# Kernel tuning notes

Hardware: AMD Instinct MI355X
Metric: run time of the kernel (lower is better)

## Reference

```python
import jax, jax.numpy as jnp
import numpy as np

LN_EPS = 1e-5


def setup_inputs() -> dict:
    key = jax.random.key(0)
    ks = jax.random.split(key, 8)
    B, S, D = 8, 2048, 1024
    scale = 1.0 / np.sqrt(D)
    return {
        "inp": jax.random.normal(ks[0], (B, S, D), dtype=jnp.float32),
        "lens": jax.random.randint(ks[1], (B,), 1, S + 1, dtype=jnp.int64),
        "Wq": jax.random.normal(ks[2], (D, D), dtype=jnp.float32) * scale,
        "bq": jnp.zeros((D,), dtype=jnp.float32),
        "Wk": jax.random.normal(ks[3], (D, D), dtype=jnp.float32) * scale,
        "bk": jnp.zeros((D,), dtype=jnp.float32),
        "Wv": jax.random.normal(ks[4], (D, D), dtype=jnp.float32) * scale,
        "bv": jnp.zeros((D,), dtype=jnp.float32),
        "ln_gamma": jnp.ones((D,), dtype=jnp.float32),
        "ln_beta": jnp.zeros((D,), dtype=jnp.float32),
    }


def reference(inp, lens, Wq, bq, Wk, bk, Wv, bv, ln_gamma, ln_beta):
    # inp: [B, S, D]; dk = dv = D
    B, S, D = inp.shape
    q = jnp.einsum("bsd,kd->bsk", inp, Wq) + bq  # [B, S, D]
    k = jnp.einsum("bsd,kd->bsk", inp, Wk) + bk
    v = jnp.einsum("bsd,kd->bsk", inp, Wv) + bv
    # scores[b, i, j] = q[b, i] . k[b, j]
    scores = jnp.einsum("bid,bjd->bij", q, k)  # [B, S, S]
    # NON-standard: softmax over the QUERY axis (dim=1), then divide by sqrt(dk)
    attn = jax.nn.softmax(scores, axis=1) / jnp.sqrt(jnp.asarray(D, scores.dtype))
    selfatt = jnp.einsum("bij,bjd->bid", attn, v)  # [B, S, D]
    # LayerNorm over last dim, then mean-pool over sequence (sum / seq_len)
    mu = jnp.mean(selfatt, axis=-1, keepdims=True)
    var = jnp.mean(jnp.square(selfatt - mu), axis=-1, keepdims=True)
    ln = (selfatt - mu) * jax.lax.rsqrt(var + LN_EPS) * ln_gamma + ln_beta
    context = jnp.sum(ln, axis=1) / S  # [B, D]
    return context
```

## Files before the change

kernel.cpp:

```cpp
#include <hip/hip_runtime.h>
#include <hip/hip_fp16.h>

#define B_ 8
#define S_ 2048
#define D_ 1024
#define M_ (B_ * S_)
#define NCH 8
#define LN_EPS 1e-5f

typedef _Float16 f16;
typedef _Float16 half8 __attribute__((ext_vector_type(8)));
typedef _Float16 half4_t __attribute__((ext_vector_type(4)));
typedef float floatx4 __attribute__((ext_vector_type(4)));

__device__ __forceinline__ void gload_lds16(const void* g, void* l) {
  __builtin_amdgcn_global_load_lds((const __attribute__((address_space(1))) void*)g,
                                   (__attribute__((address_space(3))) void*)l, 16, 0, 0);
}

__device__ __forceinline__ void xcd_remap(int& bx, int& by, int& bz) {
  const int gx = gridDim.x, gy = gridDim.y;
  const int nb = gx * gy * (int)gridDim.z;
  int f = blockIdx.x + gx * (blockIdx.y + gy * blockIdx.z);
  const int cpx = nb >> 3;
  f = (f & 7) * cpx + (f >> 3);
  bx = f % gx;
  f /= gx;
  by = f % gy;
  bz = f / gy;
}

__global__ void k_cvt(const float* __restrict__ src, f16* __restrict__ dst, int n4) {
  int stride = gridDim.x * blockDim.x;
  for (int i = blockIdx.x * blockDim.x + threadIdx.x; i < n4; i += stride) {
    float4 v = ((const float4*)src)[i];
    half4_t h;
    h.x = (f16)v.x; h.y = (f16)v.y; h.z = (f16)v.z; h.w = (f16)v.w;
    ((half4_t*)dst)[i] = h;
  }
}

__global__ void k_cvtw(const float* __restrict__ a, const float* __restrict__ b,
                       const float* __restrict__ c, f16* __restrict__ dst) {
  const int n4 = D_ * D_ / 4;
  const int i = blockIdx.x * 256 + threadIdx.x;
  const int which = i / n4, off = i - which * n4;
  const float* s = which == 0 ? a : (which == 1 ? b : c);
  const float4 v = ((const float4*)s)[off];
  half4_t h;
  h.x = (f16)v.x; h.y = (f16)v.y; h.z = (f16)v.z; h.w = (f16)v.w;
  ((half4_t*)dst)[i] = h;
}

#define STG_A(tn, h, buf)                                                     \
  {                                                                           \
    const f16* g = aG + (size_t)(tn) * 64 + (size_t)(h) * 128 * K;            \
    f16* l = As + (buf) * 16384 + (h) * 8192 + lOff;                          \
    gload_lds16(g, l);                                                        \
    gload_lds16(g + (size_t)64 * K, l + 4096);                                \
  }
#define STG_B(tn, h, buf)                                                     \
  {                                                                           \
    const f16* g = bG + (size_t)(tn) * 64 + (size_t)(h) * 128 * K;            \
    f16* l = Bs + (buf) * 16384 + (h) * 8192 + lOff;                          \
    gload_lds16(g, l);                                                        \
    gload_lds16(g + (size_t)64 * K, l + 4096);                                \
  }

__device__ __forceinline__ void gemm8_loop(
    const f16* aG, const f16* bG, f16* As, f16* Bs, const int K, const int lOff,
    const int wr, const int wc, const int fr, const int fs0, const int fs1,
    floatx4 (&acc)[2][4][2][2]) {
  const int NT = K >> 6;
  const int NP = NT >> 1;

  STG_A(0, 0, 0);
  STG_B(0, 0, 0);
  STG_B(0, 1, 0);
  STG_A(0, 1, 0);
  STG_A(1, 0, 1);
  STG_B(1, 0, 1);
  asm volatile("s_waitcnt vmcnt(8)" ::: "memory");
  __builtin_amdgcn_s_barrier();

  half8 af[4][2], bf0[2][2], bf1[2][2];

#define LDA(BUF, MH)                                                          \
  _Pragma("unroll") for (int m = 0; m < 4; ++m) {                             \
    const f16* Ac = As + (BUF) * 16384;                                       \
    const int ar = ((MH) * 128 + wr * 64 + m * 16 + fr) * 64;                 \
    af[m][0] = *(const half8*)(Ac + ar + fs0);                                \
    af[m][1] = *(const half8*)(Ac + ar + fs1);                                \
  }
#define LDB(BUF, NH, DST)                                                     \
  _Pragma("unroll") for (int n = 0; n < 2; ++n) {                             \
    const f16* Bc = Bs + (BUF) * 16384;                                       \
    const int br = ((NH) * 128 + wc * 32 + n * 16 + fr) * 64;                 \
    DST[n][0] = *(const half8*)(Bc + br + fs0);                               \
    DST[n][1] = *(const half8*)(Bc + br + fs1);                               \
  }
#define PH(LOADS, MH, NH, BF, STAGE_STMT, WAIT_STMT)                          \
  {                                                                           \
    LOADS;                                                                    \
    STAGE_STMT;                                                               \
    __builtin_amdgcn_s_barrier();                                             \
    __builtin_amdgcn_s_setprio(1);                                            \
    _Pragma("unroll") for (int m = 0; m < 4; ++m)                             \
      _Pragma("unroll") for (int n = 0; n < 2; ++n)                           \
        _Pragma("unroll") for (int kk = 0; kk < 2; ++kk)                      \
          acc[MH][m][NH][n] = __builtin_amdgcn_mfma_f32_16x16x32_f16(         \
              af[m][kk], BF[n][kk], acc[MH][m][NH][n], 0, 0, 0);              \
    __builtin_amdgcn_s_setprio(0);                                            \
    WAIT_STMT;                                                                \
    __builtin_amdgcn_s_barrier();                                             \
  }
#define VW8 asm volatile("s_waitcnt vmcnt(8)" ::: "memory")
#define VW4 asm volatile("s_waitcnt vmcnt(4)" ::: "memory")
#define VW2 asm volatile("s_waitcnt vmcnt(2)" ::: "memory")
#define VW0 asm volatile("s_waitcnt vmcnt(0)" ::: "memory")

  for (int p = 0; p < NP; ++p) {
    const int t0 = 2 * p;
    const bool mid = (t0 + 2 < NT);
    const bool nxt = (t0 + 3 < NT);
    const bool last = (p == NP - 1);

    PH(LDA(0, 0); LDB(0, 0, bf0), 0, 0, bf0, STG_B(t0 + 1, 1, 1), VW8);
    PH(LDB(0, 1, bf1), 0, 1, bf1, STG_A(t0 + 1, 1, 1), VW8);
    PH(LDA(0, 1), 1, 1, bf1, if (mid) STG_A(t0 + 2, 0, 0), VW8);
    PH((void)0, 1, 0, bf0, if (mid) STG_B(t0 + 2, 0, 0),
       if (last) { VW4; } else { VW8; });
    PH(LDA(1, 0); LDB(1, 0, bf0), 0, 0, bf0, if (mid) STG_B(t0 + 2, 1, 0),
       if (last) { VW2; } else { VW8; });
    PH(LDB(1, 1, bf1), 0, 1, bf1, if (mid) STG_A(t0 + 2, 1, 0),
       if (last) { VW0; } else { VW8; });
    PH(LDA(1, 1), 1, 1, bf1, if (nxt) STG_A(t0 + 3, 0, 1), VW8);
    PH((void)0, 1, 0, bf0, if (nxt) STG_B(t0 + 3, 0, 1), VW8);
  }
#undef PH
#undef LDA
#undef LDB
#undef VW8
#undef VW4
#undef VW2
#undef VW0
}

template <bool OUTF16, bool BIAS>
__global__ __launch_bounds__(512, 2) void k_gemm8(
    const f16* __restrict__ A, const f16* __restrict__ Bm, void* __restrict__ Cv,
    const float* __restrict__ bias, const int K, const int N,
    const long sA, const long sB, const long sC) {
  __shared__ f16 As[2 * 256 * 64];
  __shared__ f16 Bs[2 * 256 * 64];
  int bx, by, bz;
  xcd_remap(bx, by, bz);
  const int tid = threadIdx.x;
  const int wid = tid >> 6, lane = tid & 63;
  const int wr = wid >> 2, wc = wid & 3;
  const int fr = lane & 15;

  const f16* Ab = A + (size_t)bz * sA + (size_t)by * 256 * K;
  const f16* Bb = Bm + (size_t)bz * sB + (size_t)bx * 256 * K;
  const int srow = tid >> 3;
  const int sslot = (tid & 7) ^ (srow & 7);
  const f16* aG = Ab + (size_t)srow * K + sslot * 8;
  const f16* bG = Bb + (size_t)srow * K + sslot * 8;
  const int lOff = srow * 64 + (tid & 7) * 8;

  const int sx = lane & 7;
  const int fs0 = (((lane >> 4)) ^ sx) * 8;
  const int fs1 = ((4 + (lane >> 4)) ^ sx) * 8;

  floatx4 acc[2][4][2][2] = {};
  gemm8_loop(aG, bG, As, Bs, K, lOff, wr, wc, fr, fs0, fs1, acc);

#pragma unroll
  for (int mh = 0; mh < 2; ++mh)
#pragma unroll
    for (int m = 0; m < 4; ++m) {
      const int row0 = by * 256 + mh * 128 + wr * 64 + m * 16 + (lane >> 4) * 4;
#pragma unroll
      for (int nh = 0; nh < 2; ++nh)
#pragma unroll
        for (int n = 0; n < 2; ++n) {
          const int col = bx * 256 + nh * 128 + wc * 32 + n * 16 + (lane & 15);
          float bv = 0.0f;
          if constexpr (BIAS) bv = bias[col];
#pragma unroll
          for (int r = 0; r < 4; ++r) {
            const float v = acc[mh][m][nh][n][r] + bv;
            if constexpr (OUTF16)
              ((f16*)Cv)[(size_t)bz * sC + (size_t)(row0 + r) * N + col] = (f16)v;
            else
              ((float*)Cv)[(size_t)bz * sC + (size_t)(row0 + r) * N + col] = v;
          }
        }
    }
}

__global__ __launch_bounds__(512, 2) void k_scores8(
    const f16* __restrict__ Q, const f16* __restrict__ Kx, f16* __restrict__ Sc,
    float* __restrict__ pm, float* __restrict__ pz) {
  __shared__ f16 As[2 * 256 * 64];
  __shared__ f16 Bs[2 * 256 * 64];
  __shared__ float smax[2][256];
  __shared__ float ssum[2][256];
  int bx, by, bz;
  xcd_remap(bx, by, bz);
  const int tid = threadIdx.x;
  const int wid = tid >> 6, lane = tid & 63;
  const int wr = wid >> 2, wc = wid & 3;
  const int fr = lane & 15;
  const int K = D_;

  const f16* Ab = Q + (size_t)bz * S_ * D_ + (size_t)by * 256 * K;
  const f16* Bb = Kx + (size_t)bz * S_ * D_ + (size_t)bx * 256 * K;
  const int srow = tid >> 3;
  const int sslot = (tid & 7) ^ (srow & 7);
  const f16* aG = Ab + (size_t)srow * K + sslot * 8;
  const f16* bG = Bb + (size_t)srow * K + sslot * 8;
  const int lOff = srow * 64 + (tid & 7) * 8;

  const int sx = lane & 7;
  const int fs0 = (((lane >> 4)) ^ sx) * 8;
  const int fs1 = ((4 + (lane >> 4)) ^ sx) * 8;

  floatx4 acc[2][4][2][2] = {};
  gemm8_loop(aG, bG, As, Bs, K, lOff, wr, wc, fr, fs0, fs1, acc);

#pragma unroll
  for (int mh = 0; mh < 2; ++mh)
#pragma unroll
    for (int m = 0; m < 4; ++m) {
      const int row0 = by * 256 + mh * 128 + wr * 64 + m * 16 + (lane >> 4) * 4;
#pragma unroll
      for (int nh = 0; nh < 2; ++nh)
#pragma unroll
        for (int n = 0; n < 2; ++n) {
          const int col = bx * 256 + nh * 128 + wc * 32 + n * 16 + fr;
#pragma unroll
          for (int r = 0; r < 4; ++r)
            Sc[(size_t)bz * S_ * S_ + (size_t)(row0 + r) * S_ + col] =
                (f16)acc[mh][m][nh][n][r];
        }
    }

  float cmax[2][2], csum[2][2];
#pragma unroll
  for (int nh = 0; nh < 2; ++nh)
#pragma unroll
    for (int n = 0; n < 2; ++n) {
      float mx = -1e30f;
#pragma unroll
      for (int mh = 0; mh < 2; ++mh)
#pragma unroll
        for (int m = 0; m < 4; ++m)
#pragma unroll
          for (int r = 0; r < 4; ++r)
            mx = fmaxf(mx, (float)(f16)acc[mh][m][nh][n][r]);
      float zz = 0.f;
#pragma unroll
      for (int mh = 0; mh < 2; ++mh)
#pragma unroll
        for (int m = 0; m < 4; ++m)
#pragma unroll
          for (int r = 0; r < 4; ++r)
            zz += __expf((float)(f16)acc[mh][m][nh][n][r] - mx);
#pragma unroll
      for (int o = 16; o <= 32; o <<= 1) {
        const float om = __shfl_xor(mx, o);
        const float oz = __shfl_xor(zz, o);
        const float nm = fmaxf(mx, om);
        zz = zz * __expf(mx - nm) + oz * __expf(om - nm);
        mx = nm;
      }
      cmax[nh][n] = mx;
      csum[nh][n] = zz;
    }
  __syncthreads();
  if ((lane >> 4) == 0) {
#pragma unroll
    for (int nh = 0; nh < 2; ++nh)
#pragma unroll
      for (int n = 0; n < 2; ++n) {
        const int c = nh * 128 + wc * 32 + n * 16 + fr;
        smax[wr][c] = cmax[nh][n];
        ssum[wr][c] = csum[nh][n];
      }
  }
  __syncthreads();
  if (wr == 0 && (lane >> 4) == 0) {
#pragma unroll
    for (int nh = 0; nh < 2; ++nh)
#pragma unroll
      for (int n = 0; n < 2; ++n) {
        const int c = nh * 128 + wc * 32 + n * 16 + fr;
        const float m0 = smax[0][c], m1 = smax[1][c];
        const float nm = fmaxf(m0, m1);
        const float zz = ssum[0][c] * __expf(m0 - nm) + ssum[1][c] * __expf(m1 - nm);
        const size_t o = ((size_t)bz * NCH + by) * S_ + bx * 256 + c;
        pm[o] = nm;
        pz[o] = zz;
      }
  }
}

__global__ void k_combine(const float* __restrict__ pm, const float* __restrict__ pz,
                          float* __restrict__ mcol, float* __restrict__ cscale) {
  const int b = blockIdx.y;
  const int j = blockIdx.x * 256 + threadIdx.x;
  float m = -1e30f;
#pragma unroll
  for (int ch = 0; ch < NCH; ++ch) m = fmaxf(m, pm[((size_t)b * NCH + ch) * S_ + j]);
  float z = 0.f;
#pragma unroll
  for (int ch = 0; ch < NCH; ++ch)
    z += pz[((size_t)b * NCH + ch) * S_ + j] * __expf(pm[((size_t)b * NCH + ch) * S_ + j] - m);
  mcol[(size_t)b * S_ + j] = m;
  cscale[(size_t)b * S_ + j] = 1.0f / (z * 32.0f);
}

__global__ void k_pexp16(f16* __restrict__ P, const float* __restrict__ mcol,
                         const float* __restrict__ cscale) {
  const int n4 = B_ * S_ * S_ / 4;
  const int stride = gridDim.x * blockDim.x;
  for (int i = blockIdx.x * blockDim.x + threadIdx.x; i < n4; i += stride) {
    const size_t e = (size_t)i * 4;
    const int z = (int)(e / ((size_t)S_ * S_));
    const int j = (int)(e & (S_ - 1));
    const half4_t s4 = ((const half4_t*)P)[i];
    const float4 mv = *(const float4*)(mcol + (size_t)z * S_ + j);
    const float4 cv = *(const float4*)(cscale + (size_t)z * S_ + j);
    half4_t h;
    h.x = (f16)(__expf((float)s4.x - mv.x) * cv.x);
    h.y = (f16)(__expf((float)s4.y - mv.y) * cv.y);
    h.z = (f16)(__expf((float)s4.z - mv.z) * cv.z);
    h.w = (f16)(__expf((float)s4.w - mv.w) * cv.w);
    ((half4_t*)P)[i] = h;
  }
}

__global__ void k_transpose(const f16* __restrict__ V, f16* __restrict__ Vt) {
  __shared__ f16 t[64][72];
  const int b = blockIdx.z;
  const int j0 = blockIdx.x * 64, d0 = blockIdx.y * 64;
  const int rr = threadIdx.x >> 4;
  const int cc = (threadIdx.x & 15) * 4;
#pragma unroll
  for (int p = 0; p < 4; ++p) {
    const int j = rr + p * 16;
    const half4_t v = *(const half4_t*)(V + ((size_t)b * S_ + j0 + j) * D_ + d0 + cc);
    *(half4_t*)&t[j][cc] = v;
  }
  __syncthreads();
#pragma unroll
  for (int p = 0; p < 4; ++p) {
    const int d = rr + p * 16;
    half4_t v;
    v.x = t[cc][d]; v.y = t[cc + 1][d]; v.z = t[cc + 2][d]; v.w = t[cc + 3][d];
    *(half4_t*)(Vt + ((size_t)b * D_ + d0 + d) * S_ + j0 + cc) = v;
  }
}

__global__ __launch_bounds__(256) void k_ln_pool(
    const f16* __restrict__ selfatt, const float* __restrict__ gamma,
    const float* __restrict__ beta, float* __restrict__ part) {
  __shared__ float lds[4 * 1024];
  const int tid = threadIdx.x, wid = tid >> 6, lane = tid & 63;
  const int row0 = blockIdx.x * 64 + wid * 16;
  float g[16], be[16], acc[16];
#pragma unroll
  for (int t = 0; t < 16; ++t) {
    g[t] = gamma[lane + 64 * t];
    be[t] = beta[lane + 64 * t];
    acc[t] = 0.f;
  }
  for (int r = 0; r < 16; ++r) {
    const f16* xp = selfatt + (size_t)(row0 + r) * D_ + lane;
    float x[16], sum = 0.f, sq = 0.f;
#pragma unroll
    for (int t = 0; t < 16; ++t) {
      x[t] = (float)xp[64 * t];
      sum += x[t];
      sq += x[t] * x[t];
    }
#pragma unroll
    for (int o = 32; o > 0; o >>= 1) {
      sum += __shfl_xor(sum, o);
      sq += __shfl_xor(sq, o);
    }
    const float mu = sum * (1.f / 1024.f);
    const float var = sq * (1.f / 1024.f) - mu * mu;
    const float rstd = rsqrtf(var + LN_EPS);
#pragma unroll
    for (int t = 0; t < 16; ++t) acc[t] += (x[t] - mu) * rstd * g[t] + be[t];
  }
#pragma unroll
  for (int t = 0; t < 16; ++t) lds[wid * 1024 + lane + 64 * t] = acc[t];
  __syncthreads();
#pragma unroll
  for (int c = 0; c < 4; ++c) {
    const int d = tid + 256 * c;
    const float s = lds[d] + lds[1024 + d] + lds[2048 + d] + lds[3072 + d];
    part[(size_t)blockIdx.x * 1024 + d] = s;
  }
}

__global__ void k_final(const float* __restrict__ part, float* __restrict__ out) {
  const int idx = blockIdx.x * 256 + threadIdx.x;
  const int b = idx >> 10, d = idx & 1023;
  float s = 0.f;
#pragma unroll
  for (int slot = 0; slot < 32; ++slot)
    s += part[((size_t)(b * 32 + slot)) * 1024 + d];
  out[idx] = s * (1.0f / S_);
}

extern "C" void kernel_launch(void* const* d_in, const int* in_sizes, int n_in,
                              void* d_out, int out_size, void* d_ws, size_t ws_size,
                              hipStream_t stream) {
  (void)in_sizes; (void)n_in; (void)out_size;
  const float* inp = (const float*)d_in[0];
  const float* Wq = (const float*)d_in[2];
  const float* bq = (const float*)d_in[3];
  const float* Wk = (const float*)d_in[4];
  const float* bk = (const float*)d_in[5];
  const float* Wv = (const float*)d_in[6];
  const float* bv = (const float*)d_in[7];
  const float* gamma = (const float*)d_in[8];
  const float* beta = (const float*)d_in[9];
  float* out = (float*)d_out;

  char* ws = (char*)d_ws;
  const size_t MB = 1024 * 1024;
  if (ws_size < 244 * MB) return;

  f16* Xh = (f16*)(ws);
  f16* Qh = (f16*)(ws + 32 * MB);
  f16* Kh = (f16*)(ws + 64 * MB);
  f16* Vh = (f16*)(ws + 96 * MB);
  f16* Vt = (f16*)(ws + 128 * MB);
  f16* Sc = (f16*)(ws + 160 * MB);
  f16* Wh = (f16*)(ws + 224 * MB);
  float* pm = (float*)(ws + 230 * MB);
  float* pz = (float*)(ws + 231 * MB);
  float* mcol = (float*)(ws + 232 * MB);
  float* cscale = mcol + (size_t)B_ * S_;
  float* part = (float*)(ws + 233 * MB);
  f16* selfatt = Xh;

  k_cvt<<<2048, 256, 0, stream>>>(inp, Xh, M_ * D_ / 4);
  k_cvtw<<<3 * D_ * D_ / 4 / 256, 256, 0, stream>>>(Wq, Wk, Wv, Wh);

  dim3 gp8(D_ / 256, M_ / 256, 1);
  k_gemm8<true, true><<<gp8, 512, 0, stream>>>(Xh, Wh, Qh, bq, D_, D_, 0, 0, 0);
  k_gemm8<true, true><<<gp8, 512, 0, stream>>>(Xh, Wh + D_ * D_, Kh, bk, D_, D_, 0, 0, 0);
  k_gemm8<true, true><<<gp8, 512, 0, stream>>>(Xh, Wh + 2 * D_ * D_, Vh, bv, D_, D_, 0, 0, 0);

  k_transpose<<<dim3(S_ / 64, D_ / 64, B_), 256, 0, stream>>>(Vh, Vt);

  k_scores8<<<dim3(S_ / 256, S_ / 256, B_), 512, 0, stream>>>(Qh, Kh, Sc, pm, pz);
  k_combine<<<dim3(S_ / 256, B_), 256, 0, stream>>>(pm, pz, mcol, cscale);
  k_pexp16<<<2048, 256, 0, stream>>>(Sc, mcol, cscale);

  k_gemm8<true, false><<<dim3(D_ / 256, S_ / 256, B_), 512, 0, stream>>>(
      Sc, Vt, selfatt, nullptr, S_, D_,
      (long)S_ * S_, (long)D_ * S_, (long)S_ * D_);

  k_ln_pool<<<M_ / 64, 256, 0, stream>>>(selfatt, gamma, beta, part);
  k_final<<<(B_ * D_) / 256, 256, 0, stream>>>(part, out);
}
```

Measured before the change: 329.5 us.

## Fuse QKV projections into one GEMM launch and relax vmcnt waits

```diff
diff --git a/kernel.cpp b/kernel.cpp
--- a/kernel.cpp
+++ b/kernel.cpp
@@ -80,7 +80,7 @@
   STG_A(0, 1, 0);
   STG_A(1, 0, 1);
   STG_B(1, 0, 1);
-  asm volatile("s_waitcnt vmcnt(8)" ::: "memory");
+  asm volatile("s_waitcnt vmcnt(4)" ::: "memory");
   __builtin_amdgcn_s_barrier();
 
   half8 af[4][2], bf0[2][2], bf1[2][2];
@@ -114,10 +114,10 @@
     WAIT_STMT;                                                                \
     __builtin_amdgcn_s_barrier();                                             \
   }
-#define VW8 asm volatile("s_waitcnt vmcnt(8)" ::: "memory")
 #define VW4 asm volatile("s_waitcnt vmcnt(4)" ::: "memory")
 #define VW2 asm volatile("s_waitcnt vmcnt(2)" ::: "memory")
 #define VW0 asm volatile("s_waitcnt vmcnt(0)" ::: "memory")
+#define NOW (void)0
 
   for (int p = 0; p < NP; ++p) {
     const int t0 = 2 * p;
@@ -125,25 +125,24 @@
     const bool nxt = (t0 + 3 < NT);
     const bool last = (p == NP - 1);
 
-    PH(LDA(0, 0); LDB(0, 0, bf0), 0, 0, bf0, STG_B(t0 + 1, 1, 1), VW8);
-    PH(LDB(0, 1, bf1), 0, 1, bf1, STG_A(t0 + 1, 1, 1), VW8);
-    PH(LDA(0, 1), 1, 1, bf1, if (mid) STG_A(t0 + 2, 0, 0), VW8);
-    PH((void)0, 1, 0, bf0, if (mid) STG_B(t0 + 2, 0, 0),
-       if (last) { VW4; } else { VW8; });
+    PH(LDA(0, 0); LDB(0, 0, bf0), 0, 0, bf0, STG_B(t0 + 1, 1, 1), NOW);
+    PH(LDB(0, 1, bf1), 0, 1, bf1, STG_A(t0 + 1, 1, 1), NOW);
+    PH(LDA(0, 1), 1, 1, bf1, if (mid) STG_A(t0 + 2, 0, 0), NOW);
+    PH(NOW, 1, 0, bf0, if (mid) STG_B(t0 + 2, 0, 0), VW4);
     PH(LDA(1, 0); LDB(1, 0, bf0), 0, 0, bf0, if (mid) STG_B(t0 + 2, 1, 0),
-       if (last) { VW2; } else { VW8; });
+       if (last) { VW2; });
     PH(LDB(1, 1, bf1), 0, 1, bf1, if (mid) STG_A(t0 + 2, 1, 0),
-       if (last) { VW0; } else { VW8; });
-    PH(LDA(1, 1), 1, 1, bf1, if (nxt) STG_A(t0 + 3, 0, 1), VW8);
-    PH((void)0, 1, 0, bf0, if (nxt) STG_B(t0 + 3, 0, 1), VW8);
+       if (last) { VW0; });
+    PH(LDA(1, 1), 1, 1, bf1, if (nxt) STG_A(t0 + 3, 0, 1), NOW);
+    PH(NOW, 1, 0, bf0, if (nxt) STG_B(t0 + 3, 0, 1), if (!last) { VW4; });
   }
 #undef PH
 #undef LDA
 #undef LDB
-#undef VW8
 #undef VW4
 #undef VW2
 #undef VW0
+#undef NOW
 }
 
 template <bool OUTF16, bool BIAS>
@@ -195,6 +194,59 @@
             else
               ((float*)Cv)[(size_t)bz * sC + (size_t)(row0 + r) * N + col] = v;
           }
+        }
+    }
+}
+
+__global__ __launch_bounds__(512, 2) void k_qkv8(
+    const f16* __restrict__ X, const f16* __restrict__ W,
+    f16* __restrict__ Qh, f16* __restrict__ Kh, f16* __restrict__ Vh,
+    const float* __restrict__ bq, const float* __restrict__ bk,
+    const float* __restrict__ bv) {
+  __shared__ f16 As[2 * 256 * 64];
+  __shared__ f16 Bs[2 * 256 * 64];
+  int bx, by, bz;
+  xcd_remap(bx, by, bz);
+  (void)bz;
+  const int K = D_;
+  const int tid = threadIdx.x;
+  const int wid = tid >> 6, lane = tid & 63;
+  const int wr = wid >> 2, wc = wid & 3;
+  const int fr = lane & 15;
+
+  const f16* Ab = X + (size_t)by * 256 * K;
+  const f16* Bb = W + (size_t)bx * 256 * K;
+  const int srow = tid >> 3;
+  const int sslot = (tid & 7) ^ (srow & 7);
+  const f16* aG = Ab + (size_t)srow * K + sslot * 8;
+  const f16* bG = Bb + (size_t)srow * K + sslot * 8;
+  const int lOff = srow * 64 + (tid & 7) * 8;
+
+  const int sx = lane & 7;
+  const int fs0 = (((lane >> 4)) ^ sx) * 8;
+  const int fs1 = ((4 + (lane >> 4)) ^ sx) * 8;
+
+  floatx4 acc[2][4][2][2] = {};
+  gemm8_loop(aG, bG, As, Bs, K, lOff, wr, wc, fr, fs0, fs1, acc);
+
+#pragma unroll
+  for (int mh = 0; mh < 2; ++mh)
+#pragma unroll
+    for (int m = 0; m < 4; ++m) {
+      const int row0 = mh * 128 + wr * 64 + m * 16 + (lane >> 4) * 4 + by * 256;
+#pragma unroll
+      for (int nh = 0; nh < 2; ++nh)
+#pragma unroll
+        for (int n = 0; n < 2; ++n) {
+          const int col = bx * 256 + nh * 128 + wc * 32 + n * 16 + (lane & 15);
+          const int which = col >> 10;
+          const int lcol = col & 1023;
+          f16* outp = which == 0 ? Qh : (which == 1 ? Kh : Vh);
+          const float* bp = which == 0 ? bq : (which == 1 ? bk : bv);
+          const float bvv = bp[lcol];
+#pragma unroll
+          for (int r = 0; r < 4; ++r)
+            outp[(size_t)(row0 + r) * D_ + lcol] = (f16)(acc[mh][m][nh][n][r] + bvv);
         }
     }
 }
@@ -453,10 +505,8 @@
   k_cvt<<<2048, 256, 0, stream>>>(inp, Xh, M_ * D_ / 4);
   k_cvtw<<<3 * D_ * D_ / 4 / 256, 256, 0, stream>>>(Wq, Wk, Wv, Wh);
 
-  dim3 gp8(D_ / 256, M_ / 256, 1);
-  k_gemm8<true, true><<<gp8, 512, 0, stream>>>(Xh, Wh, Qh, bq, D_, D_, 0, 0, 0);
-  k_gemm8<true, true><<<gp8, 512, 0, stream>>>(Xh, Wh + D_ * D_, Kh, bk, D_, D_, 0, 0, 0);
-  k_gemm8<true, true><<<gp8, 512, 0, stream>>>(Xh, Wh + 2 * D_ * D_, Vh, bv, D_, D_, 0, 0, 0);
+  k_qkv8<<<dim3(3 * D_ / 256, M_ / 256, 1), 512, 0, stream>>>(
+      Xh, Wh, Qh, Kh, Vh, bq, bk, bv);
 
   k_transpose<<<dim3(S_ / 64, D_ / 64, B_), 256, 0, stream>>>(Vh, Vt);
 
```

New measurement: 319.0 us. 3.2% less time.
